# Performance work log

Hardware: AMD Instinct MI355X
Metric: run time of the kernel (lower is better)

## Reference

```python
import jax, jax.numpy as jnp
import numpy as np

N = 50000
E = 800000
D_IN = 96
D_OUT = 128


def setup_inputs() -> dict:
    key = jax.random.key(0)
    k1, k2, k3, k4, k5 = jax.random.split(key, 5)
    x = jax.random.normal(k1, (N, D_IN), dtype=jnp.float32)
    edge_index = jax.random.randint(k2, (2, E), 0, N, dtype=jnp.int32)
    s = 1.0 / np.sqrt(D_IN)
    # lin_l: applied to aggregated neighbor features (has bias in PyG SAGEConv)
    W_l = jax.random.uniform(k3, (D_OUT, D_IN), jnp.float32, -s, s)
    b_l = jax.random.uniform(k4, (D_OUT,), jnp.float32, -s, s)
    # lin_r: root/self weight (no bias)
    W_r = jax.random.uniform(k5, (D_OUT, D_IN), jnp.float32, -s, s)
    return {"x": x, "edge_index": edge_index, "W_l": W_l, "b_l": b_l, "W_r": W_r}


def reference(x, edge_index, W_l, b_l, W_r):
    src, dst = edge_index[0], edge_index[1]
    # gather source features, mean-aggregate onto targets
    msg = x[src]  # [E, D_IN]
    summed = jax.ops.segment_sum(msg, dst, num_segments=N)  # [N, D_IN]
    count = jax.ops.segment_sum(jnp.ones((E,), x.dtype), dst, num_segments=N)
    agg = summed / jnp.maximum(count, 1.0)[:, None]
    # SAGEConv: lin_l(agg) + lin_r(x), then layer-level ReLU
    out = agg @ W_l.T + b_l + x @ W_r.T
    return jax.nn.relu(out)
```

## Files before the change

### kernel.cpp

```cpp
#include <hip/hip_runtime.h>
#include <hip/hip_bf16.h>

#define N_NODES 50000
#define N_EDGES 800000
#define D_IN 96
#define D_OUT 128
#define CAP 64
#define CAPP 72

#define NPB 50
#define N_BINS ((N_NODES + NPB - 1) / NPB)
#define CAP_SUB 24
#define CAP_STRIDE 32
#define PART_EPB 3125
#define PART_BLOCKS (N_EDGES / PART_EPB)
#define PART_SLOTS 13

#define CONV_THREADS (N_NODES * 12)
#define CONV_BLOCKS ((CONV_THREADS + 255) / 256)
#define WCONV_BLOCKS 12

#define AG_BLOCKS N_BINS
#define AH_PITCH 104

typedef unsigned short u16;
typedef __attribute__((ext_vector_type(8))) short short8;
typedef __attribute__((ext_vector_type(4))) float f32x4;

__device__ __forceinline__ u16 f2bf(float f) {
    unsigned u = __float_as_uint(f);
    unsigned r = (u + 0x7FFFu + ((u >> 16) & 1u)) >> 16;
    return (u16)r;
}
__device__ __forceinline__ float bf2f(u16 h) {
    return __uint_as_float(((unsigned)h) << 16);
}

__global__ __launch_bounds__(256) void sage_part_conv(
    const int* __restrict__ src,
    const int* __restrict__ dst,
    const float* __restrict__ x,
    const float* __restrict__ Wl,
    const float* __restrict__ Wr,
    u16* __restrict__ cnts,
    unsigned* __restrict__ binbuf,
    u16* __restrict__ xh,
    u16* __restrict__ Wfrag)
{
    __shared__ unsigned hist[N_BINS];
    __shared__ unsigned cur[N_BINS];

    const int b = blockIdx.x;
    const int tid = (int)threadIdx.x;

    if (b < PART_BLOCKS) {
        for (int i = tid; i < N_BINS; i += 256) { hist[i] = 0u; cur[i] = 0u; }
        __syncthreads();

        const int ebase = b * PART_EPB;
        const int e0 = ebase + tid;
        int d[PART_SLOTS], s[PART_SLOTS];
#pragma unroll
        for (int i = 0; i < PART_SLOTS; i++) {
            int valid = (tid + i * 256) < PART_EPB;
            int e = valid ? (e0 + i * 256) : ebase;
            d[i] = dst[e];
            s[i] = src[e];
        }
#pragma unroll
        for (int i = 0; i < PART_SLOTS; i++) {
            if ((tid + i * 256) < PART_EPB)
                atomicAdd(&hist[d[i] / NPB], 1u);
        }
        __syncthreads();
        for (int i = tid; i < N_BINS; i += 256)
            cnts[(size_t)i * PART_BLOCKS + b] = (u16)hist[i];
#pragma unroll
        for (int i = 0; i < PART_SLOTS; i++) {
            if ((tid + i * 256) < PART_EPB) {
                int bn = d[i] / NPB;
                unsigned dl = (unsigned)(d[i] - bn * NPB);
                unsigned loc = atomicAdd(&cur[bn], 1u);
                if (loc < CAP_SUB)
                    binbuf[((unsigned)bn * PART_BLOCKS + (unsigned)b) * CAP_STRIDE
                           + loc] = (dl << 16) | (unsigned)s[i];
            }
        }
    } else if (b < PART_BLOCKS + CONV_BLOCKS) {
        unsigned t = (unsigned)(b - PART_BLOCKS) * 256u + threadIdx.x;
        if (t >= (unsigned)CONV_THREADS) return;
        unsigned n = t / 12u;
        unsigned c8 = t - n * 12u;
        const float* p = x + (size_t)n * D_IN + c8 * 8u;
        short8 v;
#pragma unroll
        for (int i = 0; i < 8; i++) v[i] = (short)f2bf(p[i]);
        *(short8*)(xh + (size_t)n * D_IN + c8 * 8u) = v;
    } else {
        int idx = (b - PART_BLOCKS - CONV_BLOCKS) * 256 + tid;
        int j = idx / 24;
        int c8 = idx - j * 24;
        int kc = c8 >> 2;
        int quad = c8 & 3;
        const float* wsrc = (c8 < 12) ? (Wl + (size_t)j * D_IN + c8 * 8)
                                      : (Wr + (size_t)j * D_IN + (c8 - 12) * 8);
        int jt = j >> 4;
        int col = j & 15;
        short8 v;
#pragma unroll
        for (int i = 0; i < 8; i++) v[i] = (short)f2bf(wsrc[i]);
        *(short8*)(Wfrag + (((jt * 6 + kc) * 64) + col + 16 * quad) * 8) = v;
    }
}

__global__ __launch_bounds__(512) void sage_agg_gemm(
    const u16* __restrict__ xh,
    const u16* __restrict__ cnts,
    const unsigned* __restrict__ binbuf,
    const u16* __restrict__ Wfrag,
    const float* __restrict__ bl,
    float* __restrict__ out)
{
    __shared__ __align__(16) u16 bkt[NPB * CAPP];
    __shared__ unsigned cnt_l[NPB];
    __shared__ __align__(16) u16 Ah[NPB * AH_PITCH];

    const int j = blockIdx.x;
    const int tid = (int)threadIdx.x;
    const int n0 = j * NPB;

    if (tid < NPB) cnt_l[tid] = 0u;
    __syncthreads();

    if (tid < PART_BLOCKS) {
        unsigned cnt_t = cnts[(size_t)j * PART_BLOCKS + tid];
        const uint4* sc = (const uint4*)(binbuf
                          + ((size_t)j * PART_BLOCKS + tid) * CAP_STRIDE);
        unsigned lim = cnt_t < CAP_SUB ? cnt_t : CAP_SUB;
        uint4 q0 = {0,0,0,0}, q1 = {0,0,0,0}, q2 = {0,0,0,0};
        uint4 q3 = {0,0,0,0}, q4 = {0,0,0,0}, q5 = {0,0,0,0};
        if (lim > 0)  q0 = sc[0];
        if (lim > 4)  q1 = sc[1];
        if (lim > 8)  q2 = sc[2];
        if (lim > 12) q3 = sc[3];
        if (lim > 16) q4 = sc[4];
        if (lim > 20) q5 = sc[5];
        unsigned buf[CAP_SUB];
        buf[0]=q0.x;  buf[1]=q0.y;  buf[2]=q0.z;  buf[3]=q0.w;
        buf[4]=q1.x;  buf[5]=q1.y;  buf[6]=q1.z;  buf[7]=q1.w;
        buf[8]=q2.x;  buf[9]=q2.y;  buf[10]=q2.z; buf[11]=q2.w;
        buf[12]=q3.x; buf[13]=q3.y; buf[14]=q3.z; buf[15]=q3.w;
        buf[16]=q4.x; buf[17]=q4.y; buf[18]=q4.z; buf[19]=q4.w;
        buf[20]=q5.x; buf[21]=q5.y; buf[22]=q5.z; buf[23]=q5.w;
#pragma unroll
        for (int e = 0; e < CAP_SUB; e++) {
            if ((unsigned)e < lim) {
                unsigned w = buf[e];
                unsigned r = w >> 16;
                unsigned p = atomicAdd(&cnt_l[r], 1u);
                if (p < CAP) bkt[r * CAPP + p] = (u16)(w & 0xFFFFu);
            }
        }
    }
    __syncthreads();

#pragma unroll
    for (int rep = 0; rep < 3; rep++) {
        int pair = rep * 256 + (tid >> 1);
        int m = pair / 12;
        int c8 = pair - m * 12;
        int half = tid & 1;

        float acc[8];
#pragma unroll
        for (int i = 0; i < 8; i++) acc[i] = 0.0f;
        int deg = 0;

        if (m < NPB) {
            deg = (int)cnt_l[m];
            int dc = deg < CAP ? deg : CAP;
            int mid = ((dc >> 1) + 4) & ~7;
            int e_lo = half ? mid : 0;
            int e_hi = half ? dc : mid;
            const u16* brow = bkt + m * CAPP;
            int e = e_lo;
            for (; e + 8 <= e_hi; e += 8) {
                short8 id = *(const short8*)(brow + e);
                short8 v[8];
#pragma unroll
                for (int q = 0; q < 8; q++) {
                    unsigned s = (u16)id[q];
                    v[q] = *(const short8*)(xh + s * (unsigned)D_IN + c8 * 8u);
                }
#pragma unroll
                for (int q = 0; q < 8; q++)
#pragma unroll
                    for (int i = 0; i < 8; i++) acc[i] += bf2f((u16)v[q][i]);
            }
            if (e + 4 <= e_hi) {
                unsigned s0 = brow[e + 0];
                unsigned s1 = brow[e + 1];
                unsigned s2 = brow[e + 2];
                unsigned s3 = brow[e + 3];
                short8 v0 = *(const short8*)(xh + s0 * (unsigned)D_IN + c8 * 8u);
                short8 v1 = *(const short8*)(xh + s1 * (unsigned)D_IN + c8 * 8u);
                short8 v2 = *(const short8*)(xh + s2 * (unsigned)D_IN + c8 * 8u);
                short8 v3 = *(const short8*)(xh + s3 * (unsigned)D_IN + c8 * 8u);
#pragma unroll
                for (int i = 0; i < 8; i++)
                    acc[i] += bf2f((u16)v0[i]) + bf2f((u16)v1[i])
                            + bf2f((u16)v2[i]) + bf2f((u16)v3[i]);
                e += 4;
            }
            for (; e < e_hi; e++) {
                unsigned s = brow[e];
                short8 v = *(const short8*)(xh + s * (unsigned)D_IN + c8 * 8u);
#pragma unroll
                for (int i = 0; i < 8; i++) acc[i] += bf2f((u16)v[i]);
            }
        }

#pragma unroll
        for (int i = 0; i < 8; i++)
            acc[i] += __shfl_xor(acc[i], 1);

        if (half == 0 && m < NPB) {
            float invd = 1.0f / fmaxf((float)deg, 1.0f);
            short8 o;
#pragma unroll
            for (int i = 0; i < 8; i++)
                o[i] = (short)f2bf(acc[i] * invd);
            *(short8*)(Ah + m * AH_PITCH + c8 * 8) = o;
        }
    }
    __syncthreads();

    const int wave = tid >> 6;
    const int lane = tid & 63;
    const int m16 = lane & 15;
    const int quad = lane >> 4;
    const int tile = wave & 3;
    const int jt0 = (wave >> 2) * 4;

    int mrow = tile * 16 + m16;
    int mclamp = mrow < NPB ? mrow : NPB - 1;
    int nn = n0 + mclamp;

    const u16* arow = Ah + mclamp * AH_PITCH + quad * 8;
    const u16* xrow = xh + (size_t)nn * D_IN + quad * 8;
    short8 a[6];
#pragma unroll
    for (int kc = 0; kc < 3; kc++) a[kc]     = *(const short8*)(arow + kc * 32);
#pragma unroll
    for (int kc = 0; kc < 3; kc++) a[3 + kc] = *(const short8*)(xrow + kc * 32);

#pragma unroll
    for (int jt = 0; jt < 4; jt++) {
        const int jtt = jt0 + jt;
        f32x4 acc = {0.0f, 0.0f, 0.0f, 0.0f};
#pragma unroll
        for (int kc = 0; kc < 6; kc++) {
            short8 bfrag = *(const short8*)(Wfrag + ((jtt * 6 + kc) * 64 + lane) * 8);
            acc = __builtin_amdgcn_mfma_f32_16x16x32_bf16(a[kc], bfrag, acc, 0, 0, 0);
        }
        const int jj = jtt * 16 + m16;
        const float bj = bl[jj];
#pragma unroll
        for (int r = 0; r < 4; r++) {
            int row = tile * 16 + quad * 4 + r;
            if (row < NPB)
                out[(size_t)(n0 + row) * D_OUT + jj] = fmaxf(acc[r] + bj, 0.0f);
        }
    }
}

extern "C" void kernel_launch(void* const* d_in, const int* in_sizes, int n_in,
                              void* d_out, int out_size, void* d_ws, size_t ws_size,
                              hipStream_t stream) {
    const float* x   = (const float*)d_in[0];
    const int* eidx  = (const int*)d_in[1];
    const float* Wl  = (const float*)d_in[2];
    const float* bl  = (const float*)d_in[3];
    const float* Wr  = (const float*)d_in[4];
    float* out = (float*)d_out;

    const int* src = eidx;
    const int* dst = eidx + N_EDGES;

    char* ws = (char*)d_ws;
    unsigned* binbuf = (unsigned*)ws;
    u16*      cnts   = (u16*)(ws + 32768000);
    u16*      xh     = (u16*)(ws + 33280000);
    u16*      Wfrag  = (u16*)(ws + 42880000);

    {
        dim3 grid(PART_BLOCKS + CONV_BLOCKS + WCONV_BLOCKS);
        sage_part_conv<<<grid, 256, 0, stream>>>(src, dst, x, Wl, Wr,
                                                 cnts, binbuf, xh, Wfrag);
    }
    {
        dim3 grid(AG_BLOCKS);
        sage_agg_gemm<<<grid, 512, 0, stream>>>(xh, cnts, binbuf,
                                                Wfrag, bl, out);
    }
}
```

Baseline: 129.2 us.

## Replace fixed-capacity padded edge bins with per-block compacted sorted edge lists

```diff
diff --git a/kernel.cpp b/kernel.cpp
--- a/kernel.cpp
+++ b/kernel.cpp
@@ -10,8 +10,7 @@
 
 #define NPB 50
 #define N_BINS ((N_NODES + NPB - 1) / NPB)
-#define CAP_SUB 24
-#define CAP_STRIDE 32
+#define NB_PAD 1024
 #define PART_EPB 3125
 #define PART_BLOCKS (N_EDGES / PART_EPB)
 #define PART_SLOTS 13
@@ -43,18 +42,22 @@
     const float* __restrict__ Wl,
     const float* __restrict__ Wr,
     u16* __restrict__ cnts,
-    unsigned* __restrict__ binbuf,
+    u16* __restrict__ offs,
+    unsigned* __restrict__ compact,
     u16* __restrict__ xh,
     u16* __restrict__ Wfrag)
 {
-    __shared__ unsigned hist[N_BINS];
-    __shared__ unsigned cur[N_BINS];
+    __shared__ unsigned hist[NB_PAD];
+    __shared__ unsigned cur[NB_PAD];
+    __shared__ unsigned base_l[NB_PAD];
+    __shared__ unsigned totals[256];
+    __shared__ unsigned edges_l[PART_EPB];
 
     const int b = blockIdx.x;
     const int tid = (int)threadIdx.x;
 
     if (b < PART_BLOCKS) {
-        for (int i = tid; i < N_BINS; i += 256) { hist[i] = 0u; cur[i] = 0u; }
+        for (int i = tid; i < NB_PAD; i += 256) { hist[i] = 0u; cur[i] = 0u; }
         __syncthreads();
 
         const int ebase = b * PART_EPB;
@@ -73,19 +76,45 @@
                 atomicAdd(&hist[d[i] / NPB], 1u);
         }
         __syncthreads();
-        for (int i = tid; i < N_BINS; i += 256)
-            cnts[(size_t)i * PART_BLOCKS + b] = (u16)hist[i];
+
+        unsigned s0 = hist[4 * tid + 0];
+        unsigned s1 = hist[4 * tid + 1];
+        unsigned s2 = hist[4 * tid + 2];
+        unsigned s3 = hist[4 * tid + 3];
+        totals[tid] = s0 + s1 + s2 + s3;
+        __syncthreads();
+        for (int st = 1; st < 256; st <<= 1) {
+            unsigned v = (tid >= st) ? totals[tid - st] : 0u;
+            __syncthreads();
+            totals[tid] += v;
+            __syncthreads();
+        }
+        unsigned tb = tid ? totals[tid - 1] : 0u;
+        base_l[4 * tid + 0] = tb;
+        base_l[4 * tid + 1] = tb + s0;
+        base_l[4 * tid + 2] = tb + s0 + s1;
+        base_l[4 * tid + 3] = tb + s0 + s1 + s2;
+        __syncthreads();
+
+        for (int i = tid; i < N_BINS; i += 256) {
+            cnts[(size_t)b * N_BINS + i] = (u16)hist[i];
+            offs[(size_t)b * N_BINS + i] = (u16)base_l[i];
+        }
+
 #pragma unroll
         for (int i = 0; i < PART_SLOTS; i++) {
             if ((tid + i * 256) < PART_EPB) {
                 int bn = d[i] / NPB;
                 unsigned dl = (unsigned)(d[i] - bn * NPB);
-                unsigned loc = atomicAdd(&cur[bn], 1u);
-                if (loc < CAP_SUB)
-                    binbuf[((unsigned)bn * PART_BLOCKS + (unsigned)b) * CAP_STRIDE
-                           + loc] = (dl << 16) | (unsigned)s[i];
+                unsigned pos = base_l[bn] + atomicAdd(&cur[bn], 1u);
+                if (pos < PART_EPB)
+                    edges_l[pos] = (dl << 16) | (unsigned)s[i];
             }
         }
+        __syncthreads();
+
+        for (int i = tid; i < PART_EPB; i += 256)
+            compact[(size_t)b * PART_EPB + i] = edges_l[i];
     } else if (b < PART_BLOCKS + CONV_BLOCKS) {
         unsigned t = (unsigned)(b - PART_BLOCKS) * 256u + threadIdx.x;
         if (t >= (unsigned)CONV_THREADS) return;
@@ -116,7 +145,8 @@
 __global__ __launch_bounds__(512) void sage_agg_gemm(
     const u16* __restrict__ xh,
     const u16* __restrict__ cnts,
-    const unsigned* __restrict__ binbuf,
+    const u16* __restrict__ offs,
+    const unsigned* __restrict__ compact,
     const u16* __restrict__ Wfrag,
     const float* __restrict__ bl,
     float* __restrict__ out)
@@ -133,33 +163,14 @@
     __syncthreads();
 
     if (tid < PART_BLOCKS) {
-        unsigned cnt_t = cnts[(size_t)j * PART_BLOCKS + tid];
-        const uint4* sc = (const uint4*)(binbuf
-                          + ((size_t)j * PART_BLOCKS + tid) * CAP_STRIDE);
-        unsigned lim = cnt_t < CAP_SUB ? cnt_t : CAP_SUB;
-        uint4 q0 = {0,0,0,0}, q1 = {0,0,0,0}, q2 = {0,0,0,0};
-        uint4 q3 = {0,0,0,0}, q4 = {0,0,0,0}, q5 = {0,0,0,0};
-        if (lim > 0)  q0 = sc[0];
-        if (lim > 4)  q1 = sc[1];
-        if (lim > 8)  q2 = sc[2];
-        if (lim > 12) q3 = sc[3];
-        if (lim > 16) q4 = sc[4];
-        if (lim > 20) q5 = sc[5];
-        unsigned buf[CAP_SUB];
-        buf[0]=q0.x;  buf[1]=q0.y;  buf[2]=q0.z;  buf[3]=q0.w;
-        buf[4]=q1.x;  buf[5]=q1.y;  buf[6]=q1.z;  buf[7]=q1.w;
-        buf[8]=q2.x;  buf[9]=q2.y;  buf[10]=q2.z; buf[11]=q2.w;
-        buf[12]=q3.x; buf[13]=q3.y; buf[14]=q3.z; buf[15]=q3.w;
-        buf[16]=q4.x; buf[17]=q4.y; buf[18]=q4.z; buf[19]=q4.w;
-        buf[20]=q5.x; buf[21]=q5.y; buf[22]=q5.z; buf[23]=q5.w;
-#pragma unroll
-        for (int e = 0; e < CAP_SUB; e++) {
-            if ((unsigned)e < lim) {
-                unsigned w = buf[e];
-                unsigned r = w >> 16;
-                unsigned p = atomicAdd(&cnt_l[r], 1u);
-                if (p < CAP) bkt[r * CAPP + p] = (u16)(w & 0xFFFFu);
-            }
+        unsigned cnt = cnts[(size_t)tid * N_BINS + j];
+        unsigned off = offs[(size_t)tid * N_BINS + j];
+        const unsigned* cp = compact + (size_t)tid * PART_EPB + off;
+        for (unsigned k = 0; k < cnt; k++) {
+            unsigned w = cp[k];
+            unsigned r = w >> 16;
+            unsigned p = atomicAdd(&cnt_l[r], 1u);
+            if (p < CAP) bkt[r * CAPP + p] = (u16)(w & 0xFFFFu);
         }
     }
     __syncthreads();
@@ -288,19 +299,20 @@
     const int* dst = eidx + N_EDGES;
 
     char* ws = (char*)d_ws;
-    unsigned* binbuf = (unsigned*)ws;
-    u16*      cnts   = (u16*)(ws + 32768000);
-    u16*      xh     = (u16*)(ws + 33280000);
-    u16*      Wfrag  = (u16*)(ws + 42880000);
+    unsigned* compact = (unsigned*)ws;
+    u16*      cnts    = (u16*)(ws + 12800000);
+    u16*      offs    = (u16*)(ws + 13312000);
+    u16*      xh      = (u16*)(ws + 13824000);
+    u16*      Wfrag   = (u16*)(ws + 23424000);
 
     {
         dim3 grid(PART_BLOCKS + CONV_BLOCKS + WCONV_BLOCKS);
         sage_part_conv<<<grid, 256, 0, stream>>>(src, dst, x, Wl, Wr,
-                                                 cnts, binbuf, xh, Wfrag);
+                                                 cnts, offs, compact, xh, Wfrag);
     }
     {
         dim3 grid(AG_BLOCKS);
-        sage_agg_gemm<<<grid, 512, 0, stream>>>(xh, cnts, binbuf,
+        sage_agg_gemm<<<grid, 512, 0, stream>>>(xh, cnts, offs, compact,
                                                 Wfrag, bl, out);
     }
 }
```

Result: no change. 129.9 us (+0.5%).
